# Kernel tuning notes

Measured on AMD Instinct MI355X. Metric: run time of the kernel, lower is better.

The kernel has to match this reference:

```python
import jax, jax.numpy as jnp
import numpy as np

NUM_TREES = 64
DEPTH = 11                      # complete binary trees, 2^11-1 = 2047 nodes each
H = 256                         # hidden_dim
E = 256                         # embedding_dim
V = 30000                       # vocab
C = 104                         # n_classes
NPT = 2 ** DEPTH - 1
N = NUM_TREES * NPT


def setup_inputs() -> dict:
    key = jax.random.key(0)
    ks = jax.random.split(key, 6)
    s = 0.05
    return {
        "features": jax.random.randint(ks[0], (N,), 0, V),
        "emb": jax.random.normal(ks[1], (V, E), dtype=jnp.float32) * s,
        "W_iou": jax.random.normal(ks[2], (3 * H, E), dtype=jnp.float32) * s,
        "U_iou": jax.random.normal(ks[3], (3 * H, H), dtype=jnp.float32) * s,
        "b_iou": jnp.zeros((1, 3 * H), dtype=jnp.float32),
        "U_f_w": jax.random.normal(ks[4], (H, H), dtype=jnp.float32) * s,
        "U_f_b": jnp.zeros((H,), dtype=jnp.float32),
        "lin_w": jax.random.normal(ks[5], (C, H), dtype=jnp.float32) * s,
        "lin_b": jnp.zeros((C,), dtype=jnp.float32),
        "num_trees": NUM_TREES,
        "depth": DEPTH,
    }


def reference(features, emb, W_iou, U_iou, b_iou, U_f_w, U_f_b, lin_w, lin_b,
              num_trees, depth):
    npt = 2 ** depth - 1
    n = num_trees * npt
    Hd = U_f_w.shape[0]
    x = emb[features]                          # [N, E] embedding lookup
    iou_all = x @ W_iou.T                      # [N, 3H]  W_iou(x) per node
    h = jnp.zeros((n, Hd), dtype=emb.dtype)
    c = jnp.zeros((n, Hd), dtype=emb.dtype)
    tree_off = np.arange(num_trees)[:, None] * npt  # [B,1] global node offsets
    # process topological levels bottom-up (leaves = level depth-1)
    for l in range(depth - 1, -1, -1):
        local = np.arange(2 ** l - 1, 2 ** (l + 1) - 1)          # heap layout
        ids = (tree_off + local[None, :]).reshape(-1)            # [M]
        if l == depth - 1:
            # leaves: no mailbox, c contribution is zero
            iou_n = iou_all[ids] + b_iou
            c_in = jnp.zeros((ids.shape[0], Hd), dtype=emb.dtype)
        else:
            ch_local = np.stack([2 * local + 1, 2 * local + 2], -1)  # [m,2]
            ch = (tree_off[:, :, None] + ch_local[None]).reshape(-1, 2)  # [M,2]
            h_ch = h[ch]                     # mailbox h: [M,2,H]
            c_ch = c[ch]                     # mailbox c: [M,2,H]
            h_head = h_ch.sum(1)             # sum over children
            f = jax.nn.sigmoid(h_ch @ U_f_w.T + U_f_b)   # per-child forget gate
            c_in = (f * c_ch).sum(1)
            iou_n = iou_all[ids] + h_head @ U_iou.T + b_iou
        i, o, u = jnp.split(iou_n, 3, axis=1)
        c_new = jax.nn.sigmoid(i) * jnp.tanh(u) + c_in
        h_new = jax.nn.sigmoid(o) * jnp.tanh(c_new)
        h = h.at[ids].set(h_new)
        c = c.at[ids].set(c_new)
    hg = h.reshape(num_trees, npt, Hd).mean(1)   # dgl.mean_nodes
    return hg @ lin_w.T + lin_b                  # [B, n_classes]
```

## Files before the change

kernel.cpp:

```cpp
#include <hip/hip_runtime.h>
#include <math.h>


#define NTREES 64
#define TDEPTH 11
#define NPT    2047
#define HD     256
#define H3     768
#define NCLS   104

typedef short v8s __attribute__((ext_vector_type(8)));
typedef float v4f __attribute__((ext_vector_type(4)));
typedef unsigned short u16;
typedef unsigned int   u32;

__device__ __forceinline__ float bf2f(u16 s) {
    u32 u = ((u32)s) << 16;
    return __builtin_bit_cast(float, u);
}
__device__ __forceinline__ u16 f2bf(float f) {
    u32 u = __builtin_bit_cast(u32, f);
    u = (u + 0x7FFFu + ((u >> 16) & 1u)) >> 16;
    return (u16)u;
}
__device__ __forceinline__ u32 pack2bf(float lo, float hi) {
    return (u32)f2bf(lo) | ((u32)f2bf(hi) << 16);
}
__device__ __forceinline__ float sigmoidf_(float x) {
    return 1.0f / (1.0f + __expf(-x));
}
__device__ __forceinline__ float tanhf_(float x) {
    x = fminf(fmaxf(x, -15.0f), 15.0f);
    float e = __expf(2.0f * x);
    return (e - 1.0f) / (e + 1.0f);
}

__global__ __launch_bounds__(256) void prep_weights(
    const float* __restrict__ W_iou, const float* __restrict__ U_iou,
    const float* __restrict__ U_f_w,
    u16* __restrict__ Wcat, u16* __restrict__ Uf)
{
    int tid = blockIdx.x * 256 + threadIdx.x;
    int j  = tid >> 8;
    int c0 = (tid & 255) * 2;
    float a, b;
    if (c0 < 256) { a = W_iou[j * 256 + c0];       b = W_iou[j * 256 + c0 + 1]; }
    else          { a = U_iou[j * 256 + c0 - 256]; b = U_iou[j * 256 + c0 - 255]; }
    Wcat[j * 512 + c0]     = f2bf(a);
    Wcat[j * 512 + c0 + 1] = f2bf(b);
    if (tid < 32768) {
        int jj = tid >> 7, cc = (tid & 127) * 2;
        Uf[jj * 256 + cc]     = f2bf(U_f_w[jj * 256 + cc]);
        Uf[jj * 256 + cc + 1] = f2bf(U_f_w[jj * 256 + cc + 1]);
    }
}

template<bool LEAF>
__global__ __launch_bounds__(512, 2) void level_kernel(
    const int* __restrict__ feat, const float* __restrict__ emb,
    const u16* __restrict__ Wcat, const u16* __restrict__ Uf,
    const float* __restrict__ b_iou, const float* __restrict__ U_f_b,
    const u16* __restrict__ h_prev, const float* __restrict__ c_prev,
    u16* __restrict__ h_cur, float* __restrict__ c_cur,
    float* __restrict__ hsum, int level)
{
    constexpr int XS = LEAF ? 264 : 520;
    __shared__ u16 xcat[64 * XS];
    __shared__ u16 hch_s[LEAF ? 8 : 128 * 264];

    const int tid = threadIdx.x;
    const int wv  = tid >> 6;
    const int ln  = tid & 63;
    const int g   = ln >> 4;
    const int r15 = ln & 15;
    const int m0  = blockIdx.x * 64;
    const int L   = 1 << level;

    int fidx[8];
    #pragma unroll
    for (int it = 0; it < 8; ++it) {
        const int m    = m0 + wv * 8 + it;
        const int tree = m >> level;
        const int pos  = m & (L - 1);
        fidx[it] = feat[tree * NPT + (L - 1) + pos];
    }
    #pragma unroll
    for (int it = 0; it < 8; ++it) {
        const int r = wv * 8 + it;
        const float4 v = *(const float4*)(emb + (size_t)fidx[it] * HD + ln * 4);
        uint2 o;
        o.x = pack2bf(v.x, v.y);
        o.y = pack2bf(v.z, v.w);
        *(uint2*)&xcat[r * XS + ln * 4] = o;
    }

    if constexpr (!LEAF) {
        #pragma unroll
        for (int it = 0; it < 8; ++it) {
            const int r = wv * 16 + it * 2 + (ln >> 5);
            v8s hv = *(const v8s*)(h_prev + (size_t)(2 * m0 + r) * HD + (ln & 31) * 8);
            *(v8s*)&hch_s[r * 264 + (ln & 31) * 8] = hv;
        }
    }
    __syncthreads();

    v4f acc2[2][8];
    if constexpr (!LEAF) {
        #pragma unroll
        for (int it = 0; it < 8; ++it) {
            const int r = wv * 8 + it;
            const uint2 a = *(const uint2*)&hch_s[(2 * r) * 264 + ln * 4];
            const uint2 b = *(const uint2*)&hch_s[(2 * r + 1) * 264 + ln * 4];
            uint2 o;
            o.x = pack2bf(bf2f(a.x & 0xffff) + bf2f(b.x & 0xffff),
                          bf2f(a.x >> 16)    + bf2f(b.x >> 16));
            o.y = pack2bf(bf2f(a.y & 0xffff) + bf2f(b.y & 0xffff),
                          bf2f(a.y >> 16)    + bf2f(b.y >> 16));
            *(uint2*)&xcat[r * XS + 256 + ln * 4] = o;
        }

        #pragma unroll
        for (int nt = 0; nt < 2; ++nt)
            #pragma unroll
            for (int mt = 0; mt < 8; ++mt)
                acc2[nt][mt] = (v4f){0.f, 0.f, 0.f, 0.f};

        for (int ks = 0; ks < 8; ++ks) {
            v8s a2[8];
            #pragma unroll
            for (int mt = 0; mt < 8; ++mt)
                a2[mt] = *(const v8s*)&hch_s[(16 * mt + r15) * 264 + ks * 32 + g * 8];
            #pragma unroll
            for (int nt = 0; nt < 2; ++nt) {
                const int n = wv + 8 * nt;
                v8s b = *(const v8s*)(Uf + (size_t)(16 * n + r15) * 256 + ks * 32 + g * 8);
                #pragma unroll
                for (int mt = 0; mt < 8; ++mt)
                    acc2[nt][mt] = __builtin_amdgcn_mfma_f32_16x16x32_bf16(
                        a2[mt], b, acc2[nt][mt], 0, 0, 0);
            }
        }
    }
    __syncthreads();

    float* cin = (float*)hch_s;
    if constexpr (!LEAF) {
        #pragma unroll
        for (int nt = 0; nt < 2; ++nt) {
            const int ch = 16 * (wv + 8 * nt) + r15;
            const float fb = U_f_b[ch];
            #pragma unroll
            for (int mt = 0; mt < 8; ++mt) {
                float ps = 0.f;
                #pragma unroll
                for (int r = 0; r < 4; ++r) {
                    const int cr = 16 * mt + 4 * g + r;
                    const float f = sigmoidf_(acc2[nt][mt][r] + fb);
                    const float cp = c_prev[(size_t)(2 * m0 + cr) * HD + ch];
                    ps = (r & 1) ? (ps + f * cp) : (f * cp);
                    if (r & 1) cin[(8 * mt + 2 * g + (r >> 1)) * 264 + ch] = ps;
                }
            }
        }
    }

    v4f acc1[6][4];
    #pragma unroll
    for (int t = 0; t < 6; ++t)
        #pragma unroll
        for (int mt = 0; mt < 4; ++mt)
            acc1[t][mt] = (v4f){0.f, 0.f, 0.f, 0.f};

    constexpr int KS1 = LEAF ? 8 : 16;
    for (int ks = 0; ks < KS1; ++ks) {
        v8s a1[4];
        #pragma unroll
        for (int mt = 0; mt < 4; ++mt)
            a1[mt] = *(const v8s*)&xcat[(16 * mt + r15) * XS + ks * 32 + g * 8];
        #pragma unroll
        for (int t = 0; t < 6; ++t) {
            const int n = wv + 8 * t;
            v8s b = *(const v8s*)(Wcat + (size_t)(16 * n + r15) * 512 + ks * 32 + g * 8);
            #pragma unroll
            for (int mt = 0; mt < 4; ++mt)
                acc1[t][mt] = __builtin_amdgcn_mfma_f32_16x16x32_bf16(
                    a1[mt], b, acc1[t][mt], 0, 0, 0);
        }
    }
    __syncthreads();

    #pragma unroll
    for (int p = 0; p < 2; ++p) {
        const int ch = 16 * (wv + 8 * p) + r15;
        const float bi = b_iou[ch];
        const float bo = b_iou[256 + ch];
        const float bu = b_iou[512 + ch];
        float hacc = 0.f;
        #pragma unroll
        for (int mt = 0; mt < 4; ++mt) {
            #pragma unroll
            for (int r = 0; r < 4; ++r) {
                const int ml = 16 * mt + 4 * g + r;
                const float iv = sigmoidf_(acc1[p][mt][r] + bi);
                const float ov = sigmoidf_(acc1[p + 2][mt][r] + bo);
                const float uv = tanhf_(acc1[p + 4][mt][r] + bu);
                float ci;
                if constexpr (LEAF) ci = 0.f;
                else ci = cin[ml * 264 + ch];
                const float cn = fmaf(iv, uv, ci);
                const float hn = ov * tanhf_(cn);
                const size_t m = (size_t)(m0 + ml);
                h_cur[m * HD + ch] = f2bf(hn);
                c_cur[m * HD + ch] = cn;
                if (level >= 6) hacc += hn;
                else atomicAdd(&hsum[((m0 + ml) >> level) * HD + ch], hn);
            }
        }
        if (level >= 6) atomicAdd(&hsum[(m0 >> level) * HD + ch], hacc);
    }
}

__global__ __launch_bounds__(128) void final_kernel(
    const float* __restrict__ hsum, const float* __restrict__ lin_w,
    const float* __restrict__ lin_b, float* __restrict__ out)
{
    __shared__ float hg[HD];
    const int tree = blockIdx.x;
    for (int j = threadIdx.x; j < HD; j += 128)
        hg[j] = hsum[tree * HD + j] * (1.0f / (float)NPT);
    __syncthreads();
    const int c = threadIdx.x;
    if (c < NCLS) {
        const float* wr = lin_w + (size_t)c * HD;
        float acc = lin_b[c];
        #pragma unroll 4
        for (int j = 0; j < HD; ++j)
            acc = fmaf(hg[j], wr[j], acc);
        out[tree * NCLS + c] = acc;
    }
}

extern "C" void kernel_launch(void* const* d_in, const int* in_sizes, int n_in,
                              void* d_out, int out_size, void* d_ws, size_t ws_size,
                              hipStream_t stream)
{
    const int*   feat  = (const int*)d_in[0];
    const float* emb   = (const float*)d_in[1];
    const float* W_iou = (const float*)d_in[2];
    const float* U_iou = (const float*)d_in[3];
    const float* b_iou = (const float*)d_in[4];
    const float* U_f_w = (const float*)d_in[5];
    const float* U_f_b = (const float*)d_in[6];
    const float* lin_w = (const float*)d_in[7];
    const float* lin_b = (const float*)d_in[8];
    float* out = (float*)d_out;

    char* ws = (char*)d_ws;
    size_t off = 0;
    auto alloc = [&](size_t bytes) -> void* {
        void* p = ws + off;
        off += (bytes + 255) & ~(size_t)255;
        return p;
    };
    u16*   Wcat = (u16*)alloc((size_t)H3 * 512 * 2);
    u16*   Uf   = (u16*)alloc((size_t)HD * HD * 2);
    float* hsum = (float*)alloc((size_t)NTREES * HD * 4);
    u16*   hA   = (u16*)alloc((size_t)65536 * HD * 2);
    u16*   hB   = (u16*)alloc((size_t)32768 * HD * 2);
    float* cA   = (float*)alloc((size_t)65536 * HD * 4);
    float* cB   = (float*)alloc((size_t)32768 * HD * 4);
    (void)ws_size; (void)in_sizes; (void)n_in; (void)out_size;

    prep_weights<<<768, 256, 0, stream>>>(W_iou, U_iou, U_f_w, Wcat, Uf);
    hipMemsetAsync(hsum, 0, (size_t)NTREES * HD * 4, stream);

    for (int l = TDEPTH - 1; l >= 0; --l) {
        const int blocks = 1 << l;
        const int p      = (TDEPTH - 1 - l) & 1;
        u16*   hc = p ? hB : hA;
        float* cc = p ? cB : cA;
        const u16*   hp = p ? hA : hB;
        const float* cp = p ? cA : cB;
        if (l == TDEPTH - 1) {
            level_kernel<true><<<blocks, 512, 0, stream>>>(
                feat, emb, Wcat, Uf, b_iou, U_f_b,
                nullptr, nullptr, hc, cc, hsum, l);
        } else {
            level_kernel<false><<<blocks, 512, 0, stream>>>(
                feat, emb, Wcat, Uf, b_iou, U_f_b,
                hp, cp, hc, cc, hsum, l);
        }
    }

    final_kernel<<<NTREES, 128, 0, stream>>>(hsum, lin_w, lin_b, out);
}
```

Before: 704.5 us.

## Drop child-h LDS staging, keep c_in in registers via shuffles, split iou GEMM

Removes the 128-row shared-memory buffer for child hidden states. The forget-gate MFMA now reads its operands straight from global memory, and c_in stays in registers, redistributed with cross-lane shuffles instead of an LDS round trip. The iou GEMM is split into two passes of three tiles so fewer accumulators are live at once, and launch bounds rise to 4 blocks per CU. Sigmoid and tanh switch to fast rcp-based forms and a library bf16 conversion. The aim is lower LDS use and register pressure for higher occupancy, at the cost of repeated global loads of h_prev and a second pass over xcat.

```diff
diff --git a/kernel.cpp b/kernel.cpp
--- a/kernel.cpp
+++ b/kernel.cpp
@@ -1,4 +1,5 @@
 #include <hip/hip_runtime.h>
+#include <hip/hip_bf16.h>
 #include <math.h>
 
 
@@ -14,25 +15,23 @@
 typedef unsigned short u16;
 typedef unsigned int   u32;
 
-__device__ __forceinline__ float bf2f(u16 s) {
-    u32 u = ((u32)s) << 16;
-    return __builtin_bit_cast(float, u);
+__device__ __forceinline__ float bfLo(u32 u) {
+    return __builtin_bit_cast(float, u << 16);
+}
+__device__ __forceinline__ float bfHi(u32 u) {
+    return __builtin_bit_cast(float, u & 0xffff0000u);
 }
 __device__ __forceinline__ u16 f2bf(float f) {
-    u32 u = __builtin_bit_cast(u32, f);
-    u = (u + 0x7FFFu + ((u >> 16) & 1u)) >> 16;
-    return (u16)u;
-}
-__device__ __forceinline__ u32 pack2bf(float lo, float hi) {
+    return __builtin_bit_cast(u16, __float2bfloat16(f));
+}
+__device__ __forceinline__ u32 pk2(float lo, float hi) {
     return (u32)f2bf(lo) | ((u32)f2bf(hi) << 16);
 }
-__device__ __forceinline__ float sigmoidf_(float x) {
-    return 1.0f / (1.0f + __expf(-x));
-}
-__device__ __forceinline__ float tanhf_(float x) {
-    x = fminf(fmaxf(x, -15.0f), 15.0f);
-    float e = __expf(2.0f * x);
-    return (e - 1.0f) / (e + 1.0f);
+__device__ __forceinline__ float sigm_(float x) {
+    return __builtin_amdgcn_rcpf(1.0f + __expf(-x));
+}
+__device__ __forceinline__ float tanh_(float x) {
+    return 1.0f - 2.0f * __builtin_amdgcn_rcpf(__expf(2.0f * x) + 1.0f);
 }
 
 __global__ __launch_bounds__(256) void prep_weights(
@@ -41,22 +40,20 @@
     u16* __restrict__ Wcat, u16* __restrict__ Uf)
 {
     int tid = blockIdx.x * 256 + threadIdx.x;
-    int j  = tid >> 8;
+    int n  = tid >> 8;
     int c0 = (tid & 255) * 2;
     float a, b;
-    if (c0 < 256) { a = W_iou[j * 256 + c0];       b = W_iou[j * 256 + c0 + 1]; }
-    else          { a = U_iou[j * 256 + c0 - 256]; b = U_iou[j * 256 + c0 - 255]; }
-    Wcat[j * 512 + c0]     = f2bf(a);
-    Wcat[j * 512 + c0 + 1] = f2bf(b);
+    if (c0 < 256) { a = W_iou[n * 256 + c0];       b = W_iou[n * 256 + c0 + 1]; }
+    else          { a = U_iou[n * 256 + c0 - 256]; b = U_iou[n * 256 + c0 - 255]; }
+    *(u32*)&Wcat[n * 512 + c0] = pk2(a, b);
     if (tid < 32768) {
         int jj = tid >> 7, cc = (tid & 127) * 2;
-        Uf[jj * 256 + cc]     = f2bf(U_f_w[jj * 256 + cc]);
-        Uf[jj * 256 + cc + 1] = f2bf(U_f_w[jj * 256 + cc + 1]);
+        *(u32*)&Uf[jj * 256 + cc] = pk2(U_f_w[jj * 256 + cc], U_f_w[jj * 256 + cc + 1]);
     }
 }
 
 template<bool LEAF>
-__global__ __launch_bounds__(512, 2) void level_kernel(
+__global__ __launch_bounds__(512, 4) void level_kernel(
     const int* __restrict__ feat, const float* __restrict__ emb,
     const u16* __restrict__ Wcat, const u16* __restrict__ Uf,
     const float* __restrict__ b_iou, const float* __restrict__ U_f_b,
@@ -66,7 +63,6 @@
 {
     constexpr int XS = LEAF ? 264 : 520;
     __shared__ u16 xcat[64 * XS];
-    __shared__ u16 hch_s[LEAF ? 8 : 128 * 264];
 
     const int tid = threadIdx.x;
     const int wv  = tid >> 6;
@@ -89,108 +85,87 @@
         const int r = wv * 8 + it;
         const float4 v = *(const float4*)(emb + (size_t)fidx[it] * HD + ln * 4);
         uint2 o;
-        o.x = pack2bf(v.x, v.y);
-        o.y = pack2bf(v.z, v.w);
+        o.x = pk2(v.x, v.y);
+        o.y = pk2(v.z, v.w);
         *(uint2*)&xcat[r * XS + ln * 4] = o;
     }
 
-    if constexpr (!LEAF) {
-        #pragma unroll
-        for (int it = 0; it < 8; ++it) {
-            const int r = wv * 16 + it * 2 + (ln >> 5);
-            v8s hv = *(const v8s*)(h_prev + (size_t)(2 * m0 + r) * HD + (ln & 31) * 8);
-            *(v8s*)&hch_s[r * 264 + (ln & 31) * 8] = hv;
-        }
-    }
-    __syncthreads();
-
-    v4f acc2[2][8];
     if constexpr (!LEAF) {
         #pragma unroll
         for (int it = 0; it < 8; ++it) {
             const int r = wv * 8 + it;
-            const uint2 a = *(const uint2*)&hch_s[(2 * r) * 264 + ln * 4];
-            const uint2 b = *(const uint2*)&hch_s[(2 * r + 1) * 264 + ln * 4];
+            const int m = m0 + r;
+            const uint2 a = *(const uint2*)(h_prev + (size_t)(2 * m) * HD + ln * 4);
+            const uint2 b = *(const uint2*)(h_prev + (size_t)(2 * m + 1) * HD + ln * 4);
             uint2 o;
-            o.x = pack2bf(bf2f(a.x & 0xffff) + bf2f(b.x & 0xffff),
-                          bf2f(a.x >> 16)    + bf2f(b.x >> 16));
-            o.y = pack2bf(bf2f(a.y & 0xffff) + bf2f(b.y & 0xffff),
-                          bf2f(a.y >> 16)    + bf2f(b.y >> 16));
+            o.x = pk2(bfLo(a.x) + bfLo(b.x), bfHi(a.x) + bfHi(b.x));
+            o.y = pk2(bfLo(a.y) + bfLo(b.y), bfHi(a.y) + bfHi(b.y));
             *(uint2*)&xcat[r * XS + 256 + ln * 4] = o;
         }
-
-        #pragma unroll
-        for (int nt = 0; nt < 2; ++nt)
-            #pragma unroll
-            for (int mt = 0; mt < 8; ++mt)
-                acc2[nt][mt] = (v4f){0.f, 0.f, 0.f, 0.f};
-
-        for (int ks = 0; ks < 8; ++ks) {
-            v8s a2[8];
-            #pragma unroll
-            for (int mt = 0; mt < 8; ++mt)
-                a2[mt] = *(const v8s*)&hch_s[(16 * mt + r15) * 264 + ks * 32 + g * 8];
-            #pragma unroll
-            for (int nt = 0; nt < 2; ++nt) {
-                const int n = wv + 8 * nt;
-                v8s b = *(const v8s*)(Uf + (size_t)(16 * n + r15) * 256 + ks * 32 + g * 8);
+    }
+    __syncthreads();
+
+    float cinreg[2][8][2];
+    if constexpr (!LEAF) {
+        const u16* hbase = h_prev + (size_t)(2 * m0) * HD;
+        #pragma unroll
+        for (int nt = 0; nt < 2; ++nt) {
+            v4f acc2[8];
+            #pragma unroll
+            for (int mt = 0; mt < 8; ++mt) acc2[mt] = (v4f){0.f, 0.f, 0.f, 0.f};
+            const int n2 = wv + 8 * nt;
+            for (int ks = 0; ks < 8; ++ks) {
+                v8s a2[8];
                 #pragma unroll
                 for (int mt = 0; mt < 8; ++mt)
-                    acc2[nt][mt] = __builtin_amdgcn_mfma_f32_16x16x32_bf16(
-                        a2[mt], b, acc2[nt][mt], 0, 0, 0);
-            }
-        }
-    }
-    __syncthreads();
-
-    float* cin = (float*)hch_s;
-    if constexpr (!LEAF) {
-        #pragma unroll
-        for (int nt = 0; nt < 2; ++nt) {
-            const int ch = 16 * (wv + 8 * nt) + r15;
+                    a2[mt] = *(const v8s*)(hbase + (size_t)(16 * mt + r15) * HD + ks * 32 + g * 8);
+                const v8s b = *(const v8s*)(Uf + (size_t)(16 * n2 + r15) * HD + ks * 32 + g * 8);
+                #pragma unroll
+                for (int mt = 0; mt < 8; ++mt)
+                    acc2[mt] = __builtin_amdgcn_mfma_f32_16x16x32_bf16(a2[mt], b, acc2[mt], 0, 0, 0);
+            }
+            const int ch = 16 * n2 + r15;
             const float fb = U_f_b[ch];
             #pragma unroll
             for (int mt = 0; mt < 8; ++mt) {
-                float ps = 0.f;
-                #pragma unroll
-                for (int r = 0; r < 4; ++r) {
-                    const int cr = 16 * mt + 4 * g + r;
-                    const float f = sigmoidf_(acc2[nt][mt][r] + fb);
-                    const float cp = c_prev[(size_t)(2 * m0 + cr) * HD + ch];
-                    ps = (r & 1) ? (ps + f * cp) : (f * cp);
-                    if (r & 1) cin[(8 * mt + 2 * g + (r >> 1)) * 264 + ch] = ps;
+                #pragma unroll
+                for (int q = 0; q < 2; ++q) {
+                    const int cr0 = 16 * mt + 4 * g + 2 * q;
+                    const float f0 = sigm_(acc2[mt][2 * q] + fb);
+                    const float f1 = sigm_(acc2[mt][2 * q + 1] + fb);
+                    const float c0 = c_prev[(size_t)(2 * m0 + cr0) * HD + ch];
+                    const float c1 = c_prev[(size_t)(2 * m0 + cr0 + 1) * HD + ch];
+                    cinreg[nt][mt][q] = fmaf(f0, c0, f1 * c1);
                 }
             }
         }
     }
-
-    v4f acc1[6][4];
-    #pragma unroll
-    for (int t = 0; t < 6; ++t)
-        #pragma unroll
-        for (int mt = 0; mt < 4; ++mt)
-            acc1[t][mt] = (v4f){0.f, 0.f, 0.f, 0.f};
-
-    constexpr int KS1 = LEAF ? 8 : 16;
-    for (int ks = 0; ks < KS1; ++ks) {
-        v8s a1[4];
-        #pragma unroll
-        for (int mt = 0; mt < 4; ++mt)
-            a1[mt] = *(const v8s*)&xcat[(16 * mt + r15) * XS + ks * 32 + g * 8];
-        #pragma unroll
-        for (int t = 0; t < 6; ++t) {
-            const int n = wv + 8 * t;
-            v8s b = *(const v8s*)(Wcat + (size_t)(16 * n + r15) * 512 + ks * 32 + g * 8);
-            #pragma unroll
-            for (int mt = 0; mt < 4; ++mt)
-                acc1[t][mt] = __builtin_amdgcn_mfma_f32_16x16x32_bf16(
-                    a1[mt], b, acc1[t][mt], 0, 0, 0);
-        }
-    }
-    __syncthreads();
 
     #pragma unroll
     for (int p = 0; p < 2; ++p) {
+        v4f acc1[3][4];
+        #pragma unroll
+        for (int t = 0; t < 3; ++t)
+            #pragma unroll
+            for (int mt = 0; mt < 4; ++mt)
+                acc1[t][mt] = (v4f){0.f, 0.f, 0.f, 0.f};
+
+        constexpr int KS1 = LEAF ? 8 : 16;
+        for (int ks = 0; ks < KS1; ++ks) {
+            v8s a1[4];
+            #pragma unroll
+            for (int mt = 0; mt < 4; ++mt)
+                a1[mt] = *(const v8s*)&xcat[(16 * mt + r15) * XS + ks * 32 + g * 8];
+            #pragma unroll
+            for (int t = 0; t < 3; ++t) {
+                const int n = wv + 8 * p + 16 * t;
+                const v8s b = *(const v8s*)(Wcat + (size_t)(16 * n + r15) * 512 + ks * 32 + g * 8);
+                #pragma unroll
+                for (int mt = 0; mt < 4; ++mt)
+                    acc1[t][mt] = __builtin_amdgcn_mfma_f32_16x16x32_bf16(a1[mt], b, acc1[t][mt], 0, 0, 0);
+            }
+        }
+
         const int ch = 16 * (wv + 8 * p) + r15;
         const float bi = b_iou[ch];
         const float bo = b_iou[256 + ch];
@@ -201,14 +176,18 @@
             #pragma unroll
             for (int r = 0; r < 4; ++r) {
                 const int ml = 16 * mt + 4 * g + r;
-                const float iv = sigmoidf_(acc1[p][mt][r] + bi);
-                const float ov = sigmoidf_(acc1[p + 2][mt][r] + bo);
-                const float uv = tanhf_(acc1[p + 4][mt][r] + bu);
-                float ci;
-                if constexpr (LEAF) ci = 0.f;
-                else ci = cin[ml * 264 + ch];
+                const float iv = sigm_(acc1[0][mt][r] + bi);
+                const float ov = sigm_(acc1[1][mt][r] + bo);
+                const float uv = tanh_(acc1[2][mt][r] + bu);
+                float ci = 0.f;
+                if constexpr (!LEAF) {
+                    const int src = (((4 * g + r) & 7) >> 1) * 16 + r15;
+                    const float va = __shfl(cinreg[p][2 * mt][r & 1], src, 64);
+                    const float vb = __shfl(cinreg[p][2 * mt + 1][r & 1], src, 64);
+                    ci = (g >= 2) ? vb : va;
+                }
                 const float cn = fmaf(iv, uv, ci);
-                const float hn = ov * tanhf_(cn);
+                const float hn = ov * tanh_(cn);
                 const size_t m = (size_t)(m0 + ml);
                 h_cur[m * HD + ch] = f2bf(hn);
                 c_cur[m * HD + ch] = cn;
```

Measured after the change: 1.258 ms. 78.6% more time.
